# Kernel tuning notes

Hardware: AMD Instinct MI355X
Metric: run time of the kernel (lower is better)

The kernel has to match this reference:

```python
import jax, jax.numpy as jnp
import numpy as np

# Module dims (match init_kwargs / input_specs)
V = 25        # number of graph nodes (chain skeleton)
K = 3         # max receptive-field size (neighbors incl. self), padded
CIN = 64
COUT = 64
N = 16
T = 512
TK = 3        # temporal_kernel
PAD = TK // 2 # time_pad default


def _build_graph():
    # Chain adjacency with self-links: node i <-> {i-1, i, i+1}
    A = np.zeros((V, V), np.float32)
    for i in range(V):
        A[i, i] = 1.0
        if i > 0:
            A[i, i - 1] = 1.0
        if i < V - 1:
            A[i, i + 1] = 1.0
    # Pad each node's neighbor list to K entries; mask marks real neighbors.
    idx = np.zeros((V, K), np.int32)
    mask = np.zeros((V, K), bool)
    for i in range(V):
        nb = np.where(A[i] != 0)[0]
        idx[i, : len(nb)] = nb
        mask[i, : len(nb)] = True
    return idx, mask


def setup_inputs() -> dict:
    key = jax.random.key(0)
    k_x, k_w, k_b = jax.random.split(key, 3)
    x = jax.random.normal(k_x, (N, CIN, V, T), dtype=jnp.float32)
    # One Conv2d kernel per node: [V, C_out, C_in, K, TK]; padded neighbor
    # slots are zeroed via mask inside reference().
    W = jax.random.normal(k_w, (V, COUT, CIN, K, TK), dtype=jnp.float32) * 0.05
    b = jax.random.normal(k_b, (V, COUT), dtype=jnp.float32) * 0.05
    idx_np, mask_np = _build_graph()
    return {
        "x": x,
        "W": W,
        "b": b,
        "idx": jnp.asarray(idx_np),
        "mask": jnp.asarray(mask_np),
    }


def reference(x, W, b, idx, mask):
    # x: [N, C, V, T]; W: [V, O, C, K, TK]; b: [V, O]; idx/mask: [V, K]
    Tt = x.shape[-1]
    # Zero out padded neighbor slots so padded rows contribute nothing
    # (equivalent to torch's variable-height per-node kernels).
    Wm = jnp.where(mask[:, None, None, :, None], W, 0.0)
    # Temporal zero padding (Conv2d padding=(0, time_pad))
    xp = jnp.pad(x, ((0, 0), (0, 0), (0, 0), (PAD, PAD)))
    # Batched neighbor gather: [N, C, V, K, T + 2*PAD]
    g = xp[:, :, idx, :]
    # Cross-correlation over the TK temporal taps (stride 1)
    out = jnp.zeros((x.shape[0], W.shape[1], V, Tt), dtype=x.dtype)
    for kt in range(TK):
        out = out + jnp.einsum(
            "ncvkt,vock->novt", g[..., kt : kt + Tt], Wm[..., kt]
        )
    out = out + b.T[None, :, :, None]  # per-node bias [O, V]
    return out
```

## Files before the change

### kernel.cpp

```cpp
#include <hip/hip_runtime.h>
#include <hip/hip_bf16.h>

#define NB   16
#define CINC 64
#define COUTC 64
#define NV   25
#define TLEN 512
#define KK   3
#define TKK  3

typedef short short8 __attribute__((ext_vector_type(8)));
typedef float f32x4  __attribute__((ext_vector_type(4)));
typedef float f32x16 __attribute__((ext_vector_type(16)));

#define XT_ROWS 514
#define XS_STRIDE 17408
#define NWT3BLK (NV * 9)

__device__ __forceinline__ unsigned pack_bf16(float lo, float hi) {
  __hip_bfloat16 l = __float2bfloat16(lo);
  __hip_bfloat16 h = __float2bfloat16(hi);
  unsigned short ul = *reinterpret_cast<unsigned short*>(&l);
  unsigned short uh = *reinterpret_cast<unsigned short*>(&h);
  return (unsigned)ul | ((unsigned)uh << 16);
}

__global__ __launch_bounds__(256) void prep_all(
    const float* __restrict__ x, const float* __restrict__ W,
    const unsigned char* __restrict__ mask_raw,
    __hip_bfloat16* __restrict__ Wt3, __hip_bfloat16* __restrict__ xT) {
  __shared__ float ts[64][65];
  int bid = blockIdx.x;
  if (bid < NWT3BLK) {
    int blk = bid;
    int v = blk / 9, kkt = blk % 9, k = kkt / 3, kt = kkt % 3;
    const int* mi = (const int*)mask_raw;
    int ok = 1;
    for (int i = 0; i < 18; ++i) {
      int m = mi[i];
      if (m != 0 && m != 1) ok = 0;
    }
    int m = ok ? mi[v * KK + k] : (int)(mask_raw[v * KK + k] != 0);
    const float* Wv = W + (size_t)v * COUTC * CINC * 9;
    __hip_bfloat16* dst = Wt3 + (size_t)blk * 4096;
    for (int i = threadIdx.x; i < 4096; i += 256) {
      int e     = i & 7;
      int lane  = (i >> 3) & 63;
      int ks    = (i >> 9) & 3;
      int oslab = i >> 11;
      int o = oslab * 32 + (lane & 31);
      int c = ks * 16 + 8 * (lane >> 5) + e;
      float val = m ? Wv[(o * CINC + c) * 9 + k * 3 + kt] : 0.f;
      dst[i] = __float2bfloat16(val);
    }
    return;
  }
  bid -= NWT3BLK;
  const int tb = (bid & 7) * 64;
  const int vn = bid >> 3;
  const int v  = vn % NV;
  const int n  = vn / NV;
  const int tid = threadIdx.x;
  for (int i = tid; i < 1024; i += 256) {
    int c = i >> 4, tq = (i & 15) * 4;
    float4 val = *(const float4*)(x + (((size_t)n * CINC + c) * NV + v) * TLEN + tb + tq);
    ts[c][tq + 0] = val.x;
    ts[c][tq + 1] = val.y;
    ts[c][tq + 2] = val.z;
    ts[c][tq + 3] = val.w;
  }
  __syncthreads();
  unsigned* base = (unsigned*)(xT + ((size_t)(n * NV + v) * XT_ROWS) * CINC);
  for (int i = tid; i < 2048; i += 256) {
    int c2 = i & 31, t = i >> 5;
    base[(tb + 1 + t) * 32 + c2] = pack_bf16(ts[2 * c2][t], ts[2 * c2 + 1][t]);
  }
  if (tb == 0 && tid < 32) base[tid] = 0u;
  if (tb == TLEN - 64 && tid < 32) base[513 * 32 + tid] = 0u;
}

__device__ __forceinline__ const char* slab_base(const __hip_bfloat16* xT,
                                                 int n, int vk, int tb) {
  return (const char*)xT + ((size_t)(n * NV + vk) * XT_ROWS + tb) * 128;
}

__global__ __launch_bounds__(256, 3) void lcn_mfma32(
    const __hip_bfloat16* __restrict__ xT,
    const __hip_bfloat16* __restrict__ Wt3,
    const float* __restrict__ bias,
    const int* __restrict__ idx,
    float* __restrict__ out) {
  __shared__ char xs[KK][XS_STRIDE];
  __shared__ char xs_dummy[1024];

  const int tb   = blockIdx.x * 128;
  const int n    = blockIdx.y;
  const int v    = blockIdx.z;
  const int tid  = threadIdx.x;
  const int lane = tid & 63;
  const int wave = tid >> 6;
  const int os   = wave & 1;
  const int th   = wave >> 1;
  const int hi   = lane >> 5;
  const int l31  = lane & 31;

#define LOAD_A(DST, KIDX)                                                     \
  {                                                                           \
    const short8* wb = (const short8*)Wt3 +                                   \
        ((size_t)((v * KK + (KIDX)) * TKK) * 2 + os) * 256 + lane;            \
    _Pragma("unroll") for (int kt = 0; kt < TKK; ++kt)                        \
      _Pragma("unroll") for (int ks = 0; ks < 4; ++ks)                        \
        DST[kt * 4 + ks] = wb[kt * 512 + (ks << 6)];                          \
  }

#define COMPUTE_K(CB, A)                                                      \
  _Pragma("unroll") for (int kt = 0; kt < TKK; ++kt) {                        \
    {                                                                         \
      const int r  = th * 64 + l31 + kt;                                      \
      const int sw = (r & 7) << 4;                                            \
      const int co = hi * 16;                                                 \
      const char* bp = (CB) + r * 128;                                        \
      _Pragma("unroll") for (int ks = 0; ks < 4; ++ks) {                      \
        short8 bfr = *(const short8*)(bp + ((co + 32 * ks) ^ sw));            \
        acc0 = __builtin_amdgcn_mfma_f32_32x32x16_bf16(A[kt * 4 + ks], bfr,   \
                                                       acc0, 0, 0, 0);        \
      }                                                                       \
    }                                                                         \
    {                                                                         \
      const int r  = th * 64 + 32 + l31 + kt;                                 \
      const int sw = (r & 7) << 4;                                            \
      const int co = hi * 16;                                                 \
      const char* bp = (CB) + r * 128;                                        \
      _Pragma("unroll") for (int ks = 0; ks < 4; ++ks) {                      \
        short8 bfr = *(const short8*)(bp + ((co + 32 * ks) ^ sw));            \
        acc1 = __builtin_amdgcn_mfma_f32_32x32x16_bf16(A[kt * 4 + ks], bfr,   \
                                                       acc1, 0, 0, 0);        \
      }                                                                       \
    }                                                                         \
  }

  short8 aP[12], aQ[12];
  LOAD_A(aP, 0)
  __builtin_amdgcn_sched_barrier(0);
  {
    const char* gb0 = slab_base(xT, n, idx[v * KK + 0], tb);
    const char* gb1 = slab_base(xT, n, idx[v * KK + 1], tb);
    const char* gb2 = slab_base(xT, n, idx[v * KK + 2], tb);
#pragma unroll
    for (int s = 0; s < KK; ++s) {
      const char* gb = (s == 0) ? gb0 : ((s == 1) ? gb1 : gb2);
#pragma unroll
      for (int q = 0; q < 4; ++q) {
        int c = wave + q * 4;
        int Lb = c * 1024 + lane * 16;
        int g = Lb ^ (((Lb >> 7) & 7) << 4);
        __builtin_amdgcn_global_load_lds(
            (const __attribute__((address_space(1))) void*)(gb + g),
            (__attribute__((address_space(3))) void*)(&xs[s][c * 1024]),
            16, 0, 0);
      }
      if (wave == 0) {
        int Lb = 16 * 1024 + lane * 16;
        int g = Lb ^ (((Lb >> 7) & 7) << 4);
        __builtin_amdgcn_global_load_lds(
            (const __attribute__((address_space(1))) void*)(gb + g),
            (__attribute__((address_space(3))) void*)(&xs[s][16 * 1024]),
            16, 0, 0);
      } else {
        __builtin_amdgcn_global_load_lds(
            (const __attribute__((address_space(1))) void*)(gb + lane * 16),
            (__attribute__((address_space(3))) void*)(xs_dummy),
            16, 0, 0);
      }
      __builtin_amdgcn_sched_barrier(0);
    }
  }

  f32x16 acc0 = {}, acc1 = {};

  asm volatile("s_waitcnt vmcnt(10)" ::: "memory");
  __builtin_amdgcn_s_barrier();
  __builtin_amdgcn_sched_barrier(0);
  LOAD_A(aQ, 1)
  COMPUTE_K(xs[0], aP)

  asm volatile("s_waitcnt vmcnt(17)" ::: "memory");
  __builtin_amdgcn_s_barrier();
  __builtin_amdgcn_sched_barrier(0);
  COMPUTE_K(xs[1], aQ)

  asm volatile("s_waitcnt vmcnt(12)" ::: "memory");
  __builtin_amdgcn_s_barrier();
  __builtin_amdgcn_sched_barrier(0);
  LOAD_A(aP, 2)
  COMPUTE_K(xs[2], aP)

#undef LOAD_A
#undef COMPUTE_K

  const float* bv = bias + v * COUTC;
#pragma unroll
  for (int s = 0; s < 2; ++s) {
    const f32x16& acc = s ? acc1 : acc0;
    const int t = tb + th * 64 + s * 32 + l31;
#pragma unroll
    for (int reg = 0; reg < 16; ++reg) {
      int o = os * 32 + 4 * hi + (reg & 3) + 8 * (reg >> 2);
      out[(((size_t)n * COUTC + o) * NV + v) * TLEN + t] = acc[reg] + bv[o];
    }
  }
}

__global__ void prep_mask_kernel(const int* __restrict__ mask_raw,
                                 int* __restrict__ mask_out) {
  __shared__ int fmt;
  if (threadIdx.x == 0) {
    int ok = 1;
    for (int i = 0; i < 18; ++i) {
      int m = mask_raw[i];
      if (m != 0 && m != 1) ok = 0;
    }
    fmt = ok;
  }
  __syncthreads();
  int i = threadIdx.x;
  if (i < NV * KK) {
    int m;
    if (fmt) m = mask_raw[i];
    else     m = (((const unsigned char*)mask_raw)[i] != 0) ? 1 : 0;
    mask_out[i] = m;
  }
}

__global__ void prep_wt_kernel(const float* __restrict__ W,
                               float* __restrict__ Wt) {
  int v   = blockIdx.x / 9;
  int kkt = blockIdx.x % 9;
  const float* Wv = W + (size_t)v * COUTC * CINC * 9;
  float* dst = Wt + (size_t)blockIdx.x * (CINC * COUTC);
  for (int i = threadIdx.x; i < CINC * COUTC; i += 256) {
    int c = i >> 6;
    int o = i & 63;
    dst[i] = Wv[(o * CINC + c) * 9 + kkt];
  }
}

__global__ __launch_bounds__(256, 4) void lcn_main(
    const float* __restrict__ x, const float* __restrict__ Wt,
    const float* __restrict__ b, const int* __restrict__ idx,
    const int* __restrict__ maskn, float* __restrict__ out) {
  __shared__ float xsf[CINC][66];
  __shared__ float wsh[CINC][COUTC];
  const int tb  = blockIdx.x * 64;
  const int v   = blockIdx.y;
  const int n   = blockIdx.z;
  const int tid = threadIdx.x;
  const int t0  = tid & 63;
  const int og  = tid >> 6;
  float acc[16];
#pragma unroll
  for (int j = 0; j < 16; ++j) acc[j] = 0.f;
  for (int k = 0; k < KK; ++k) {
    const int vk = idx[v * KK + k];
    const int mk = maskn[v * KK + k];
    __syncthreads();
    for (int i = tid; i < CINC * 66; i += 256) {
      int c  = i / 66;
      int tt = i - c * 66;
      int gt = tb - 1 + tt;
      float val = 0.f;
      if (mk && gt >= 0 && gt < TLEN)
        val = x[(((size_t)n * CINC + c) * NV + vk) * TLEN + gt];
      xsf[c][tt] = val;
    }
    for (int kt = 0; kt < TKK; ++kt) {
      __syncthreads();
      const float4* src =
          (const float4*)(Wt + ((size_t)(v * KK + k) * TKK + kt) * (CINC * COUTC));
      for (int i = tid; i < CINC * COUTC / 4; i += 256)
        ((float4*)wsh)[i] = src[i];
      __syncthreads();
#pragma unroll 4
      for (int c = 0; c < CINC; ++c) {
        float xv = xsf[c][t0 + kt];
        const float4* wrow = (const float4*)&wsh[c][og * 16];
#pragma unroll
        for (int j4 = 0; j4 < 4; ++j4) {
          float4 wv = wrow[j4];
          acc[j4 * 4 + 0] = fmaf(wv.x, xv, acc[j4 * 4 + 0]);
          acc[j4 * 4 + 1] = fmaf(wv.y, xv, acc[j4 * 4 + 1]);
          acc[j4 * 4 + 2] = fmaf(wv.z, xv, acc[j4 * 4 + 2]);
          acc[j4 * 4 + 3] = fmaf(wv.w, xv, acc[j4 * 4 + 3]);
        }
      }
    }
  }
#pragma unroll
  for (int j = 0; j < 16; ++j) {
    int o = og * 16 + j;
    out[(((size_t)n * COUTC + o) * NV + v) * TLEN + tb + t0] =
        acc[j] + b[v * COUTC + o];
  }
}

extern "C" void kernel_launch(void* const* d_in, const int* in_sizes, int n_in,
                              void* d_out, int out_size, void* d_ws, size_t ws_size,
                              hipStream_t stream) {
  const float* x    = (const float*)d_in[0];
  const float* W    = (const float*)d_in[1];
  const float* b    = (const float*)d_in[2];
  const int*   idx  = (const int*)d_in[3];
  const void*  mask = (const void*)d_in[4];
  float* out = (float*)d_out;

  const size_t WT3_BYTES = (size_t)NV * 9 * 4096 * sizeof(__hip_bfloat16);
  const size_t XT_BYTES  = (size_t)NB * NV * XT_ROWS * CINC * sizeof(__hip_bfloat16);
  const size_t NEED      = 512 + WT3_BYTES + XT_BYTES + 2048;

  if (ws_size >= NEED) {
    __hip_bfloat16* Wt3 = (__hip_bfloat16*)((char*)d_ws + 512);
    __hip_bfloat16* xT  = (__hip_bfloat16*)((char*)d_ws + 512 + WT3_BYTES);
    hipLaunchKernelGGL(prep_all, dim3(NWT3BLK + 8 * NV * NB), dim3(256), 0,
                       stream, x, W, (const unsigned char*)mask, Wt3, xT);
    hipLaunchKernelGGL(lcn_mfma32, dim3(TLEN / 128, NB, NV), dim3(256), 0,
                       stream, xT, Wt3, b, idx, out);
  } else {
    int*   maskn = (int*)d_ws;
    float* Wt    = (float*)((char*)d_ws + 512);
    hipLaunchKernelGGL(prep_mask_kernel, dim3(1), dim3(128), 0, stream,
                       (const int*)mask, maskn);
    hipLaunchKernelGGL(prep_wt_kernel, dim3(NV * KK * TKK), dim3(256), 0, stream,
                       W, Wt);
    hipLaunchKernelGGL(lcn_main, dim3(TLEN / 64, NV, NB), dim3(256), 0, stream,
                       x, Wt, b, idx, maskn, out);
  }
}
```

Before: 46.72 us.

## Fuse input transpose/bf16 conversion into main MFMA kernel, drop xT intermediate

Removes the separate pass that transposed x into a bf16 time-major padded buffer in workspace. The main kernel now loads fp32 x directly into registers, converts and packs to bf16, and writes the swizzled layout into LDS itself, pipelining the next neighbor's global loads under the current MFMA compute. This avoids writing and re-reading the full intermediate tensor, but each neighbor slab is re-read and re-converted per block (three neighbors times four time blocks), using more VGPRs and more VALU/LDS-store work inside the hot kernel.

```diff
diff --git a/kernel.cpp b/kernel.cpp
--- a/kernel.cpp
+++ b/kernel.cpp
@@ -10,12 +10,10 @@
 #define TKK  3
 
 typedef short short8 __attribute__((ext_vector_type(8)));
-typedef float f32x4  __attribute__((ext_vector_type(4)));
 typedef float f32x16 __attribute__((ext_vector_type(16)));
 
-#define XT_ROWS 514
-#define XS_STRIDE 17408
 #define NWT3BLK (NV * 9)
+#define XS_BYTES 16640
 
 __device__ __forceinline__ unsigned pack_bf16(float lo, float hi) {
   __hip_bfloat16 l = __float2bfloat16(lo);
@@ -25,73 +23,39 @@
   return (unsigned)ul | ((unsigned)uh << 16);
 }
 
-__global__ __launch_bounds__(256) void prep_all(
-    const float* __restrict__ x, const float* __restrict__ W,
-    const unsigned char* __restrict__ mask_raw,
-    __hip_bfloat16* __restrict__ Wt3, __hip_bfloat16* __restrict__ xT) {
-  __shared__ float ts[64][65];
-  int bid = blockIdx.x;
-  if (bid < NWT3BLK) {
-    int blk = bid;
-    int v = blk / 9, kkt = blk % 9, k = kkt / 3, kt = kkt % 3;
-    const int* mi = (const int*)mask_raw;
-    int ok = 1;
-    for (int i = 0; i < 18; ++i) {
-      int m = mi[i];
-      if (m != 0 && m != 1) ok = 0;
-    }
-    int m = ok ? mi[v * KK + k] : (int)(mask_raw[v * KK + k] != 0);
-    const float* Wv = W + (size_t)v * COUTC * CINC * 9;
-    __hip_bfloat16* dst = Wt3 + (size_t)blk * 4096;
-    for (int i = threadIdx.x; i < 4096; i += 256) {
-      int e     = i & 7;
-      int lane  = (i >> 3) & 63;
-      int ks    = (i >> 9) & 3;
-      int oslab = i >> 11;
-      int o = oslab * 32 + (lane & 31);
-      int c = ks * 16 + 8 * (lane >> 5) + e;
-      float val = m ? Wv[(o * CINC + c) * 9 + k * 3 + kt] : 0.f;
-      dst[i] = __float2bfloat16(val);
-    }
-    return;
-  }
-  bid -= NWT3BLK;
-  const int tb = (bid & 7) * 64;
-  const int vn = bid >> 3;
-  const int v  = vn % NV;
-  const int n  = vn / NV;
-  const int tid = threadIdx.x;
-  for (int i = tid; i < 1024; i += 256) {
-    int c = i >> 4, tq = (i & 15) * 4;
-    float4 val = *(const float4*)(x + (((size_t)n * CINC + c) * NV + v) * TLEN + tb + tq);
-    ts[c][tq + 0] = val.x;
-    ts[c][tq + 1] = val.y;
-    ts[c][tq + 2] = val.z;
-    ts[c][tq + 3] = val.w;
-  }
-  __syncthreads();
-  unsigned* base = (unsigned*)(xT + ((size_t)(n * NV + v) * XT_ROWS) * CINC);
-  for (int i = tid; i < 2048; i += 256) {
-    int c2 = i & 31, t = i >> 5;
-    base[(tb + 1 + t) * 32 + c2] = pack_bf16(ts[2 * c2][t], ts[2 * c2 + 1][t]);
-  }
-  if (tb == 0 && tid < 32) base[tid] = 0u;
-  if (tb == TLEN - 64 && tid < 32) base[513 * 32 + tid] = 0u;
-}
-
-__device__ __forceinline__ const char* slab_base(const __hip_bfloat16* xT,
-                                                 int n, int vk, int tb) {
-  return (const char*)xT + ((size_t)(n * NV + vk) * XT_ROWS + tb) * 128;
-}
-
-__global__ __launch_bounds__(256, 3) void lcn_mfma32(
-    const __hip_bfloat16* __restrict__ xT,
+__global__ __launch_bounds__(256) void prep_wt3(
+    const float* __restrict__ W, const unsigned char* __restrict__ mask_raw,
+    __hip_bfloat16* __restrict__ Wt3) {
+  int blk = blockIdx.x;
+  int v = blk / 9, kkt = blk % 9, k = kkt / 3, kt = kkt % 3;
+  const int* mi = (const int*)mask_raw;
+  int ok = 1;
+  for (int i = 0; i < 18; ++i) {
+    int m = mi[i];
+    if (m != 0 && m != 1) ok = 0;
+  }
+  int m = ok ? mi[v * KK + k] : (int)(mask_raw[v * KK + k] != 0);
+  const float* Wv = W + (size_t)v * COUTC * CINC * 9;
+  __hip_bfloat16* dst = Wt3 + (size_t)blk * 4096;
+  for (int i = threadIdx.x; i < 4096; i += 256) {
+    int e     = i & 7;
+    int lane  = (i >> 3) & 63;
+    int ks    = (i >> 9) & 3;
+    int oslab = i >> 11;
+    int o = oslab * 32 + (lane & 31);
+    int c = ks * 16 + 8 * (lane >> 5) + e;
+    float val = m ? Wv[(o * CINC + c) * 9 + k * 3 + kt] : 0.f;
+    dst[i] = __float2bfloat16(val);
+  }
+}
+
+__global__ __launch_bounds__(256, 3) void lcn_fused(
+    const float* __restrict__ x,
     const __hip_bfloat16* __restrict__ Wt3,
     const float* __restrict__ bias,
     const int* __restrict__ idx,
     float* __restrict__ out) {
-  __shared__ char xs[KK][XS_STRIDE];
-  __shared__ char xs_dummy[1024];
+  __shared__ char xs0[XS_BYTES], xs1[XS_BYTES], xs2[XS_BYTES];
 
   const int tb   = blockIdx.x * 128;
   const int n    = blockIdx.y;
@@ -103,6 +67,13 @@
   const int th   = wave >> 1;
   const int hi   = lane >> 5;
   const int l31  = lane & 31;
+  const int c2   = tid & 31;
+  const int slot = tid >> 5;
+  const int cA   = 2 * c2, cB = 2 * c2 + 1;
+
+  const int vk0 = idx[v * KK + 0];
+  const int vk1 = idx[v * KK + 1];
+  const int vk2 = idx[v * KK + 2];
 
 #define LOAD_A(DST, KIDX)                                                     \
   {                                                                           \
@@ -111,6 +82,43 @@
     _Pragma("unroll") for (int kt = 0; kt < TKK; ++kt)                        \
       _Pragma("unroll") for (int ks = 0; ks < 4; ++ks)                        \
         DST[kt * 4 + ks] = wb[kt * 512 + (ks << 6)];                          \
+  }
+
+#define LOAD_SLAB(SA, SB, VK)                                                 \
+  {                                                                           \
+    const float* pA = x + (((size_t)n * CINC + cA) * NV + (VK)) * TLEN;       \
+    const float* pB = x + (((size_t)n * CINC + cB) * NV + (VK)) * TLEN;       \
+    _Pragma("unroll") for (int j = 0; j < 5; ++j) {                           \
+      int q = slot + 8 * j;                                                   \
+      if (q > 33) q = 33;                                                     \
+      int gt = tb - 4 + 4 * q;                                                \
+      gt = gt < 0 ? 0 : (gt > TLEN - 4 ? TLEN - 4 : gt);                      \
+      SA[j] = *(const float4*)(pA + gt);                                      \
+      SB[j] = *(const float4*)(pB + gt);                                      \
+    }                                                                         \
+  }
+
+#define WRITE_SLAB(SA, SB, DST)                                               \
+  {                                                                           \
+    _Pragma("unroll") for (int j = 0; j < 5; ++j) {                           \
+      int q = slot + 8 * j;                                                   \
+      if (q < 34) {                                                           \
+        int gt = tb - 4 + 4 * q;                                              \
+        gt = gt < 0 ? 0 : (gt > TLEN - 4 ? TLEN - 4 : gt);                    \
+        float ea[4] = {SA[j].x, SA[j].y, SA[j].z, SA[j].w};                   \
+        float eb[4] = {SB[j].x, SB[j].y, SB[j].z, SB[j].w};                   \
+        _Pragma("unroll") for (int e = 0; e < 4; ++e) {                       \
+          int r = gt + e - tb + 1;                                            \
+          if (r >= 0 && r < 130) {                                            \
+            int ad = (r * 128 + c2 * 4) ^ ((r & 7) << 4);                     \
+            *(unsigned*)((DST) + ad) = pack_bf16(ea[e], eb[e]);               \
+          }                                                                   \
+        }                                                                     \
+      }                                                                       \
+    }                                                                         \
+    if (tb == 0 && slot == 0) *(unsigned*)((DST) + c2 * 4) = 0u;              \
+    if (tb == TLEN - 128 && slot == 1)                                        \
+      *(unsigned*)((DST) + ((129 * 128 + c2 * 4) ^ 16)) = 0u;                 \
   }
 
 #define COMPUTE_K(CB, A)                                                      \
@@ -140,62 +148,47 @@
   }
 
   short8 aP[12], aQ[12];
+  float4 sA[5], sB[5], tA[5], tB[5];
+
   LOAD_A(aP, 0)
   __builtin_amdgcn_sched_barrier(0);
-  {
-    const char* gb0 = slab_base(xT, n, idx[v * KK + 0], tb);
-    const char* gb1 = slab_base(xT, n, idx[v * KK + 1], tb);
-    const char* gb2 = slab_base(xT, n, idx[v * KK + 2], tb);
-#pragma unroll
-    for (int s = 0; s < KK; ++s) {
-      const char* gb = (s == 0) ? gb0 : ((s == 1) ? gb1 : gb2);
-#pragma unroll
-      for (int q = 0; q < 4; ++q) {
-        int c = wave + q * 4;
-        int Lb = c * 1024 + lane * 16;
-        int g = Lb ^ (((Lb >> 7) & 7) << 4);
-        __builtin_amdgcn_global_load_lds(
-            (const __attribute__((address_space(1))) void*)(gb + g),
-            (__attribute__((address_space(3))) void*)(&xs[s][c * 1024]),
-            16, 0, 0);
-      }
-      if (wave == 0) {
-        int Lb = 16 * 1024 + lane * 16;
-        int g = Lb ^ (((Lb >> 7) & 7) << 4);
-        __builtin_amdgcn_global_load_lds(
-            (const __attribute__((address_space(1))) void*)(gb + g),
-            (__attribute__((address_space(3))) void*)(&xs[s][16 * 1024]),
-            16, 0, 0);
-      } else {
-        __builtin_amdgcn_global_load_lds(
-            (const __attribute__((address_space(1))) void*)(gb + lane * 16),
-            (__attribute__((address_space(3))) void*)(xs_dummy),
-            16, 0, 0);
-      }
-      __builtin_amdgcn_sched_barrier(0);
-    }
-  }
+  LOAD_SLAB(sA, sB, vk0)
+  __builtin_amdgcn_sched_barrier(0);
+  LOAD_SLAB(tA, tB, vk1)
+  __builtin_amdgcn_sched_barrier(0);
+  asm volatile("s_waitcnt vmcnt(10)" ::: "memory");
+  WRITE_SLAB(sA, sB, xs0)
+  asm volatile("s_waitcnt lgkmcnt(0)" ::: "memory");
+  __builtin_amdgcn_s_barrier();
+  __builtin_amdgcn_sched_barrier(0);
 
   f32x16 acc0 = {}, acc1 = {};
 
-  asm volatile("s_waitcnt vmcnt(10)" ::: "memory");
+  LOAD_A(aQ, 1)
+  __builtin_amdgcn_sched_barrier(0);
+  COMPUTE_K(xs0, aP)
+  asm volatile("s_waitcnt vmcnt(12)" ::: "memory");
+  WRITE_SLAB(tA, tB, xs1)
+  asm volatile("s_waitcnt lgkmcnt(0)" ::: "memory");
   __builtin_amdgcn_s_barrier();
   __builtin_amdgcn_sched_barrier(0);
-  LOAD_A(aQ, 1)
-  COMPUTE_K(xs[0], aP)
-
-  asm volatile("s_waitcnt vmcnt(17)" ::: "memory");
+
+  LOAD_SLAB(sA, sB, vk2)
+  __builtin_amdgcn_sched_barrier(0);
+  LOAD_A(aP, 2)
+  __builtin_amdgcn_sched_barrier(0);
+  COMPUTE_K(xs1, aQ)
+  asm volatile("s_waitcnt vmcnt(12)" ::: "memory");
+  WRITE_SLAB(sA, sB, xs2)
+  asm volatile("s_waitcnt lgkmcnt(0)" ::: "memory");
   __builtin_amdgcn_s_barrier();
   __builtin_amdgcn_sched_barrier(0);
-  COMPUTE_K(xs[1], aQ)
-
-  asm volatile("s_waitcnt vmcnt(12)" ::: "memory");
-  __builtin_amdgcn_s_barrier();
-  __builtin_amdgcn_sched_barrier(0);
-  LOAD_A(aP, 2)
-  COMPUTE_K(xs[2], aP)
+
+  COMPUTE_K(xs2, aP)
 
 #undef LOAD_A
+#undef LOAD_SLAB
+#undef WRITE_SLAB
 #undef COMPUTE_K
 
   const float* bv = bias + v * COUTC;
@@ -314,16 +307,14 @@
   float* out = (float*)d_out;
 
   const size_t WT3_BYTES = (size_t)NV * 9 * 4096 * sizeof(__hip_bfloat16);
-  const size_t XT_BYTES  = (size_t)NB * NV * XT_ROWS * CINC * sizeof(__hip_bfloat16);
-  const size_t NEED      = 512 + WT3_BYTES + XT_BYTES + 2048;
+  const size_t NEED      = 512 + WT3_BYTES + 2048;
 
   if (ws_size >= NEED) {
     __hip_bfloat16* Wt3 = (__hip_bfloat16*)((char*)d_ws + 512);
-    __hip_bfloat16* xT  = (__hip_bfloat16*)((char*)d_ws + 512 + WT3_BYTES);
-    hipLaunchKernelGGL(prep_all, dim3(NWT3BLK + 8 * NV * NB), dim3(256), 0,
-                       stream, x, W, (const unsigned char*)mask, Wt3, xT);
-    hipLaunchKernelGGL(lcn_mfma32, dim3(TLEN / 128, NB, NV), dim3(256), 0,
-                       stream, xT, Wt3, b, idx, out);
+    hipLaunchKernelGGL(prep_wt3, dim3(NWT3BLK), dim3(256), 0, stream,
+                       W, (const unsigned char*)mask, Wt3);
+    hipLaunchKernelGGL(lcn_fused, dim3(TLEN / 128, NB, NV), dim3(256), 0,
+                       stream, x, Wt3, b, idx, out);
   } else {
     int*   maskn = (int*)d_ws;
     float* Wt    = (float*)((char*)d_ws + 512);
```

New measurement: 117.2 us. 2.51x slower.
